# Kernel optimization log

Hardware: AMD Instinct MI355X
Metric: run time of the kernel (lower is better)

Reference implementation:

```python
import jax, jax.numpy as jnp
import numpy as np

DIM = 128
HOP = 2
NEIGH = [12, 2]  # neighbor_num per hop
ALPHA = 0.2      # leaky-relu slope
NUM_NODE = 50000
B, S = 128, 50
STDV = 1.0 / np.sqrt(DIM)


def _leaky(x):
    return jnp.where(x >= 0, x, ALPHA * x)


def _local_agg(h, adj, a_local):
    # h: [B,S,D], adj: [B,S,S] ints in 0..4, a_local: [4,D]
    a_in = h[:, :, None, :] * h[:, None, :, :]            # [B,S,S,D]
    e = _leaky(jnp.einsum('bijd,kd->kbij', a_in, a_local))  # [4,B,S,S]
    att = jnp.full(adj.shape, -9e15, dtype=h.dtype)
    for k in range(4):
        att = jnp.where(adj == k + 1, e[k], att)
    att = jax.nn.softmax(att, axis=-1)
    return jnp.einsum('bij,bjd->bid', att, h)


def _global_agg(self_v, neigh_v, extra_v, w1, w2, w3, bias):
    # self_v: [B,N,D], neigh_v: [B,N,K,D], extra_v: [B,N,D]
    a = _leaky(jnp.einsum('bnkd,de->bnke', extra_v[:, :, None, :] * neigh_v, w1))
    a = jnp.einsum('bnke,e->bnk', a, w2)
    a = jax.nn.softmax(a, axis=-1)
    agg = jnp.einsum('bnk,bnkd->bnd', a, neigh_v)
    out = jnp.concatenate([self_v, agg], axis=-1) @ w3 + bias
    return jax.nn.relu(out)


def setup_inputs() -> dict:
    key = jax.random.key(0)
    ks = jax.random.split(key, 12)
    u = lambda k, shp: jax.random.uniform(k, shp, jnp.float32, -STDV, STDV)
    return {
        'inputs': jax.random.randint(ks[0], (B, S), 0, NUM_NODE),
        'adj': jax.random.randint(ks[1], (B, S, S), 0, 5),
        'mask_item': jnp.ones((B, S), dtype=jnp.int32),
        'item': jax.random.randint(ks[2], (B, S), 0, NUM_NODE),
        'first_adj': jax.random.randint(ks[3], (B, S * NEIGH[0]), 0, NUM_NODE),
        'adj_all': jax.random.randint(ks[4], (NUM_NODE, 2), 0, NUM_NODE),
        'embedding': u(ks[5], (NUM_NODE, DIM)),
        'a_local': u(ks[6], (4, DIM)),
        'gw1': u(ks[7], (HOP, DIM, DIM)),
        'gw2': u(ks[8], (HOP, DIM)),
        'gw3': u(ks[9], (HOP, 2 * DIM, DIM)),
        'gbias': u(ks[10], (HOP, DIM)),
    }


def reference(inputs, adj, mask_item, item, first_adj, adj_all,
              embedding, a_local, gw1, gw2, gw3, gbias):
    b, s = inputs.shape
    h = embedding[inputs]                                  # [B,S,D]
    h_local = _local_agg(h, adj, a_local)

    m = mask_item.astype(embedding.dtype)[..., None]       # [B,S,1]
    item_emb = embedding[item] * m
    sum_item = jnp.sum(item_emb, 1) / jnp.sum(m, 1)        # [B,D]
    sess = sum_item[:, None, :]                            # [B,1,D]

    # multi-hop neighbor sampling
    neigh1 = first_adj.reshape(b, s * NEIGH[0])            # [B, 600]
    neigh2 = adj_all[neigh1.reshape(-1)].reshape(b, s * NEIGH[0] * NEIGH[1])  # [B,1200]
    ev = [embedding[inputs], embedding[neigh1], embedding[neigh2]]

    for n_hop in range(HOP):
        nxt = []
        for hop in range(HOP - n_hop):
            neigh_v = ev[hop + 1].reshape(b, -1, NEIGH[hop], DIM)
            extra_v = jnp.broadcast_to(sess, (b, ev[hop].shape[1], DIM))
            nxt.append(_global_agg(ev[hop], neigh_v, extra_v,
                                   gw1[n_hop], gw2[n_hop], gw3[n_hop], gbias[n_hop]))
        ev = nxt
    h_global = ev[0].reshape(b, s, DIM)

    # dropout is identity at eval
    return h_local + h_global
```

## Files before the change

kernel.cpp:

```cpp
#include <hip/hip_runtime.h>
#include <stdint.h>

typedef unsigned short ushort_t;
typedef __attribute__((ext_vector_type(8))) short bf16x8;
typedef __attribute__((ext_vector_type(4))) float f32x4;

#define B_   128
#define S_   50
#define D_   128
#define ALPHA_ 0.2f

__device__ __forceinline__ float bf2f(ushort_t u){
  return __uint_as_float(((uint32_t)u) << 16);
}
__device__ __forceinline__ ushort_t f2bf(float f){
  uint32_t x = __float_as_uint(f);
  x = (x + 0x7fffu + ((x >> 16) & 1u)) >> 16;
  return (ushort_t)x;
}
__device__ __forceinline__ float leaky(float x){ return x >= 0.f ? x : ALPHA_*x; }

__device__ __forceinline__ int detect_flag_block(const uint32_t* __restrict__ emb_raw){
  __shared__ int flg;
  if (threadIdx.x == 0){
    int ok = 1;
    for (int i = 0; i < 64; i++){
      uint32_t lo = emb_raw[i] & 0xffffu;
      uint32_t ex = (lo >> 7) & 0xFFu;
      if (!(lo == 0u || (ex >= 64u && ex <= 126u))) ok = 0;
    }
    flg = ok;
  }
  __syncthreads();
  return flg;
}

#define NLOCAL_ 512
#define NSESS_  64
#define NCVT_   3174
#define NPREP_  48
#define CVT_BASE_   (NLOCAL_ + NSESS_)
#define PREP_BASE_  (CVT_BASE_ + NCVT_)
#define K1_GRID_    (PREP_BASE_ + NPREP_)

__global__ __launch_bounds__(256) void k1(
    const int* __restrict__ inputs, const int* __restrict__ adj,
    const int* __restrict__ item, const int* __restrict__ mask,
    const void* __restrict__ p0, const void* __restrict__ p1,
    const void* __restrict__ p2, const void* __restrict__ p3,
    const void* __restrict__ p4, const void* __restrict__ p5,
    ushort_t* __restrict__ emb_b, uint4* __restrict__ w1f, uint4* __restrict__ w3f,
    ushort_t* __restrict__ sessb, ushort_t* __restrict__ hlb, int skip_emb)
{
  int blk = blockIdx.x, tid = threadIdx.x;
  int flag = detect_flag_block((const uint32_t*)p0);

  if (blk < NLOCAL_){
    __shared__ ushort_t hS[64][136];
    __shared__ float    attS[16][68];
    __shared__ int      sids[64];
    __shared__ ushort_t alS[512];
    int b  = blk >> 2;
    int mi = blk & 3;
    if (tid < 64) sids[tid] = (tid < S_) ? inputs[b*S_ + tid] : 0;
    for (int i = tid; i < 512; i += 256)
      alS[i] = flag ? ((const ushort_t*)p1)[i] : f2bf(((const float*)p1)[i]);
    __syncthreads();
    if (flag){
      const ushort_t* e16 = (const ushort_t*)p0;
      for (int idx = tid; idx < 64*16; idx += 256){
        int j = idx >> 4, ch = idx & 15;
        uint4 v = {0u, 0u, 0u, 0u};
        if (j < S_) v = *(const uint4*)(e16 + (size_t)sids[j]*D_ + ch*8);
        *(uint4*)(&hS[j][ch*8]) = v;
      }
    } else {
      const float* ef = (const float*)p0;
      for (int idx = tid; idx < 64*32; idx += 256){
        int j = idx >> 5, ch = idx & 31;
        union { ushort_t u[4]; uint2 d2; } o;
        o.d2 = make_uint2(0u, 0u);
        if (j < S_){
          float4 v = *(const float4*)(ef + (size_t)sids[j]*D_ + ch*4);
          o.u[0]=f2bf(v.x); o.u[1]=f2bf(v.y); o.u[2]=f2bf(v.z); o.u[3]=f2bf(v.w);
        }
        *(uint2*)(&hS[j][ch*4]) = o.d2;
      }
    }
    for (int idx = tid; idx < 16*64; idx += 256)
      attS[idx >> 6][idx & 63] = -9.0e15f;
    __syncthreads();

    int lane = tid & 63, wv = tid >> 6;
    int q = lane >> 4, c = lane & 15;

    f32x4 Eacc[4];
    #pragma unroll
    for (int ni = 0; ni < 4; ni++) Eacc[ni] = (f32x4){0.f,0.f,0.f,0.f};
    #pragma unroll
    for (int kt = 0; kt < 4; kt++){
      uint4 av = *(const uint4*)(alS + wv*D_ + kt*32 + q*8);
      const uint32_t* ap = (const uint32_t*)&av;
      uint4 hv = *(const uint4*)(&hS[mi*16 + c][kt*32 + q*8]);
      const uint32_t* hp = (const uint32_t*)&hv;
      union { ushort_t u[8]; bf16x8 v; } afr;
      #pragma unroll
      for (int p = 0; p < 4; p++){
        float x0 = __uint_as_float(hp[p] << 16)         * __uint_as_float(ap[p] << 16);
        float x1 = __uint_as_float(hp[p] & 0xffff0000u) * __uint_as_float(ap[p] & 0xffff0000u);
        afr.u[2*p]   = f2bf(x0);
        afr.u[2*p+1] = f2bf(x1);
      }
      #pragma unroll
      for (int ni = 0; ni < 4; ni++){
        union { uint4 q4; bf16x8 v; } bfr;
        bfr.q4 = *(const uint4*)(&hS[ni*16 + c][kt*32 + q*8]);
        Eacc[ni] = __builtin_amdgcn_mfma_f32_16x16x32_bf16(afr.v, bfr.v, Eacc[ni], 0,0,0);
      }
    }
    const int* adjb = adj + (size_t)b*S_*S_;
    #pragma unroll
    for (int ni = 0; ni < 4; ni++){
      int j = ni*16 + c;
      #pragma unroll
      for (int r = 0; r < 4; r++){
        int i = mi*16 + q*4 + r;
        if (i < S_ && j < S_){
          int kk = adjb[i*S_ + j];
          if (kk == wv + 1) attS[q*4 + r][j] = leaky(Eacc[ni][r]);
        }
      }
    }
    __syncthreads();
    {
      int r  = tid >> 4;
      int cg = tid & 15;
      int i  = mi*16 + r;
      float v0 = attS[r][cg*4+0], v1 = attS[r][cg*4+1];
      float v2 = attS[r][cg*4+2], v3 = attS[r][cg*4+3];
      float mx = fmaxf(fmaxf(v0,v1), fmaxf(v2,v3));
      #pragma unroll
      for (int off = 1; off < 16; off <<= 1) mx = fmaxf(mx, __shfl_xor(mx, off, 16));
      float e0 = (cg*4+0 < S_) ? __expf(v0 - mx) : 0.f;
      float e1 = (cg*4+1 < S_) ? __expf(v1 - mx) : 0.f;
      float e2 = (cg*4+2 < S_) ? __expf(v2 - mx) : 0.f;
      float e3 = (cg*4+3 < S_) ? __expf(v3 - mx) : 0.f;
      float s = e0 + e1 + e2 + e3;
      #pragma unroll
      for (int off = 1; off < 16; off <<= 1) s += __shfl_xor(s, off, 16);
      float inv = (i < S_) ? 1.f / s : 0.f;
      attS[r][cg*4+0] = e0*inv;
      attS[r][cg*4+1] = e1*inv;
      attS[r][cg*4+2] = e2*inv;
      attS[r][cg*4+3] = e3*inv;
    }
    __syncthreads();
    f32x4 Pacc[2];
    Pacc[0] = (f32x4){0.f,0.f,0.f,0.f};
    Pacc[1] = (f32x4){0.f,0.f,0.f,0.f};
    #pragma unroll
    for (int kt = 0; kt < 2; kt++){
      union { ushort_t u[8]; bf16x8 v; } afr;
      const float* arow = &attS[c][kt*32 + q*8];
      #pragma unroll
      for (int j = 0; j < 8; j++) afr.u[j] = f2bf(arow[j]);
      #pragma unroll
      for (int nn = 0; nn < 2; nn++){
        int ni = 2*wv + nn;
        union { ushort_t u[8]; bf16x8 v; } bfr;
        #pragma unroll
        for (int jj = 0; jj < 8; jj++)
          bfr.u[jj] = hS[kt*32 + q*8 + jj][ni*16 + c];
        Pacc[nn] = __builtin_amdgcn_mfma_f32_16x16x32_bf16(afr.v, bfr.v, Pacc[nn], 0,0,0);
      }
    }
    #pragma unroll
    for (int nn = 0; nn < 2; nn++){
      int d = (2*wv + nn)*16 + c;
      #pragma unroll
      for (int r = 0; r < 4; r++){
        int i = mi*16 + q*4 + r;
        if (i < S_) hlb[((size_t)b*S_ + i)*D_ + d] = f2bf(Pacc[nn][r]);
      }
    }
  } else if (blk < CVT_BASE_){
    int b = (blk - NLOCAL_)*2 + (tid >> 7);
    int d = tid & 127;
    float acc = 0.f, den = 0.f;
    if (flag){
      const ushort_t* e16 = (const ushort_t*)p0;
      for (int s = 0; s < S_; s++){
        float fm = (float)mask[b*S_ + s];
        int id = item[b*S_ + s];
        acc += fm * bf2f(e16[(size_t)id*D_ + d]);
        den += fm;
      }
    } else {
      const float* ef = (const float*)p0;
      for (int s = 0; s < S_; s++){
        float fm = (float)mask[b*S_ + s];
        int id = item[b*S_ + s];
        acc += fm * ef[(size_t)id*D_ + d];
        den += fm;
      }
    }
    sessb[b*D_ + d] = f2bf(acc / den);
  } else if (blk < PREP_BASE_){
    const int seg_end[6] = {6400000, 6400512, 6433280, 6433536, 6499072, 6499328};
    int base = ((blk - CVT_BASE_)*256 + tid) * 8;
    if (base >= 6499328) return;
    if (flag && skip_emb && base < 6400000) return;
    int s = 0;
    while (base >= seg_end[s]) s++;
    int segbase = (s == 0) ? 0 : seg_end[s-1];
    const void* src = (s==0)?p0:(s==1)?p1:(s==2)?p2:(s==3)?p3:(s==4)?p4:p5;
    int off = base - segbase;
    union { ushort_t u[8]; uint4 q4; } o;
    if (flag){
      o.q4 = *(const uint4*)((const ushort_t*)src + off);
    } else {
      const float* fp = (const float*)src + off;
      float4 v0 = *(const float4*)(fp);
      float4 v1 = *(const float4*)(fp + 4);
      o.u[0]=f2bf(v0.x); o.u[1]=f2bf(v0.y); o.u[2]=f2bf(v0.z); o.u[3]=f2bf(v0.w);
      o.u[4]=f2bf(v1.x); o.u[5]=f2bf(v1.y); o.u[6]=f2bf(v1.z); o.u[7]=f2bf(v1.w);
    }
    *(uint4*)(emb_b + base) = o.q4;
  } else {
    int id = (blk - PREP_BASE_)*256 + tid;
    if (id >= 12288) return;
    if (id < 4096){
      int h = id >> 11, i = id & 2047;
      int kt = i >> 9, rem = i & 511, t = rem >> 6, ln = rem & 63;
      int q = ln >> 4, c = ln & 15;
      union { ushort_t u[8]; uint4 q4; } e;
      #pragma unroll
      for (int j = 0; j < 8; j++){
        int idx = h*16384 + (32*kt + q*8 + j)*128 + 16*t + c;
        e.u[j] = flag ? ((const ushort_t*)p2)[idx] : f2bf(((const float*)p2)[idx]);
      }
      w1f[h*2048 + i] = e.q4;
    } else {
      int id2 = id - 4096;
      int h = id2 >> 12, i = id2 & 4095;
      int kt = i >> 9, rem = i & 511, t = rem >> 6, ln = rem & 63;
      int q = ln >> 4, c = ln & 15;
      union { ushort_t u[8]; uint4 q4; } e;
      #pragma unroll
      for (int j = 0; j < 8; j++){
        int idx = h*32768 + (32*kt + q*8 + j)*128 + 16*t + c;
        e.u[j] = flag ? ((const ushort_t*)p4)[idx] : f2bf(((const float*)p4)[idx]);
      }
      w3f[h*4096 + i] = e.q4;
    }
  }
}

#define NT2SCORE_ 768
#define NT2TPREP_ 392
#define K2_GRID_  (NT2SCORE_ + NT2TPREP_)

__global__ __launch_bounds__(256) void k2(
    const void* __restrict__ p0, const ushort_t* __restrict__ emb_b,
    const uint4* __restrict__ w3f,
    ushort_t* __restrict__ Tt, ushort_t* __restrict__ Tb,
    const ushort_t* __restrict__ sessb,
    const int* __restrict__ neigh1, const int* __restrict__ adj_all,
    const uint4* __restrict__ w1f, const ushort_t* __restrict__ w2,
    float* __restrict__ score)
{
  __shared__ uint4 frag[2048];
  __shared__ ushort_t sS[128];
  int blk = blockIdx.x, tid = threadIdx.x;
  int flag = detect_flag_block((const uint32_t*)p0);
  const ushort_t* emb = flag ? (const ushort_t*)p0 : emb_b;

  if (blk >= NT2SCORE_){
    int tp   = blk - NT2SCORE_;
    int half = tp & 1;
    int rowbase0 = (tp >> 1) * 256;
    for (int i = tid; i < 2048; i += 256) frag[i] = w3f[half*2048 + i];
    __syncthreads();
    int lane = tid & 63, wave = tid >> 6;
    int m = lane & 15, q = lane >> 4;
    ushort_t* Tdst = half ? Tb : Tt;
    #pragma unroll
    for (int rit = 0; rit < 4; rit++){
      int row = rowbase0 + rit*64 + wave*16 + m;
      int rowc = row < 50000 ? row : 49999;
      f32x4 acc[8];
      #pragma unroll
      for (int t = 0; t < 8; t++) acc[t] = (f32x4){0.f,0.f,0.f,0.f};
      #pragma unroll
      for (int kt = 0; kt < 4; kt++){
        union { uint4 q4; bf16x8 v; } bfr;
        bfr.q4 = *(const uint4*)(emb + (size_t)rowc*D_ + kt*32 + q*8);
        #pragma unroll
        for (int t = 0; t < 8; t++){
          union { uint4 q4; bf16x8 v; } af;
          af.q4 = frag[(kt*8 + t)*64 + lane];
          acc[t] = __builtin_amdgcn_mfma_f32_16x16x32_bf16(af.v, bfr.v, acc[t], 0, 0, 0);
        }
      }
      if (row < 50000){
        ushort_t* dst = Tdst + (size_t)row*D_;
        #pragma unroll
        for (int t = 0; t < 8; t++){
          int col0 = 16*t + q*4;
          union { ushort_t u[4]; uint2 d2; } pk;
          #pragma unroll
          for (int r = 0; r < 4; r++) pk.u[r] = f2bf(acc[t][r]);
          *(uint2*)(dst + col0) = pk.d2;
        }
      }
    }
    return;
  }

  int b2  = blk;
  int sb  = b2 / 6;
  int sub = b2 - sb*6;
  int grp = sub >> 1;
  int halft = sub & 1;
  if (tid < 16) ((uint4*)sS)[tid] = ((const uint4*)(sessb + (size_t)sb*D_))[tid];
  __syncthreads();
  for (int i = tid; i < 2048; i += 256){
    int kt = i >> 9, ln = i & 63, q = (ln >> 4);
    uint4 w = w1f[i];
    uint4 sv = *(const uint4*)(sS + kt*32 + q*8);
    const ushort_t* wu = (const ushort_t*)&w;
    const ushort_t* su = (const ushort_t*)&sv;
    union { ushort_t u[8]; uint4 q4; } o;
    #pragma unroll
    for (int j = 0; j < 8; j++) o.u[j] = f2bf(bf2f(wu[j]) * bf2f(su[j]));
    frag[i] = o.q4;
  }
  __syncthreads();
  int lane = tid & 63, wave = tid >> 6;
  int m = lane & 15, q = lane >> 4;
  float w2v[8];
  #pragma unroll
  for (int t = 0; t < 8; t++) w2v[t] = bf2f(w2[16*t + m]);

  int tend = halft ? 38 : 19;
  for (int t = halft*19 + wave; t < tend; t += 4){
    int rr = t*16 + m;
    int rrc = rr < 599 ? rr : 599;
    int nid;
    if (grp == 0){
      nid = neigh1[sb*600 + rrc];
    } else {
      int r2 = sb*1200 + (grp-1)*600 + rrc;
      nid = adj_all[(size_t)neigh1[r2 >> 1]*2 + (r2 & 1)];
    }
    const ushort_t* nrow = emb + (size_t)nid*D_;
    f32x4 acc[8];
    #pragma unroll
    for (int t8 = 0; t8 < 8; t8++) acc[t8] = (f32x4){0.f,0.f,0.f,0.f};
    #pragma unroll
    for (int kt = 0; kt < 4; kt++){
      union { uint4 q4; bf16x8 v; } af;
      af.q4 = *(const uint4*)(nrow + kt*32 + q*8);
      #pragma unroll
      for (int t8 = 0; t8 < 8; t8++){
        union { uint4 q4; bf16x8 v; } bf;
        bf.q4 = frag[(kt*8 + t8)*64 + lane];
        acc[t8] = __builtin_amdgcn_mfma_f32_16x16x32_bf16(af.v, bf.v, acc[t8], 0, 0, 0);
      }
    }
    #pragma unroll
    for (int r = 0; r < 4; r++){
      float s = 0.f;
      #pragma unroll
      for (int t8 = 0; t8 < 8; t8++) s += leaky(acc[t8][r]) * w2v[t8];
      s += __shfl_xor(s, 1, 64);
      s += __shfl_xor(s, 2, 64);
      s += __shfl_xor(s, 4, 64);
      s += __shfl_xor(s, 8, 64);
      if (m == 0){
        int rw = t*16 + q*4 + r;
        if (rw < 600){
          int sidx = (grp == 0) ? (sb*600 + rw)
                                : (76800 + sb*1200 + (grp-1)*600 + rw);
          score[sidx] = s;
        }
      }
    }
  }
}

__global__ __launch_bounds__(256) void score2_c(
    const ushort_t* __restrict__ sessb, const ushort_t* __restrict__ out1,
    const uint4* __restrict__ w1f, const ushort_t* __restrict__ w2,
    float* __restrict__ score)
{
  __shared__ uint4 bfrag[2048];
  __shared__ ushort_t sS[128];
  int blk = blockIdx.x, tid = threadIdx.x;
  int sb  = blk >> 2;
  int qtr = blk & 3;
  if (tid < 16) ((uint4*)sS)[tid] = ((const uint4*)(sessb + (size_t)sb*D_))[tid];
  __syncthreads();
  for (int i = tid; i < 2048; i += 256){
    int kt = i >> 9, ln = i & 63, q = (ln >> 4);
    uint4 w = w1f[i];
    uint4 sv = *(const uint4*)(sS + kt*32 + q*8);
    const ushort_t* wu = (const ushort_t*)&w;
    const ushort_t* su = (const ushort_t*)&sv;
    union { ushort_t u[8]; uint4 q4; } o;
    #pragma unroll
    for (int j = 0; j < 8; j++) o.u[j] = f2bf(bf2f(wu[j]) * bf2f(su[j]));
    bfrag[i] = o.q4;
  }
  __syncthreads();
  int lane = tid & 63, wave = tid >> 6;
  int m = lane & 15, q = lane >> 4;
  float w2v[8];
  #pragma unroll
  for (int t = 0; t < 8; t++) w2v[t] = bf2f(w2[16*t + m]);

  int t0 = qtr*10, tend = (qtr*10 + 10 < 38) ? qtr*10 + 10 : 38;
  for (int t = t0 + wave; t < tend; t += 4){
    int rr = t*16 + m;
    int rrc = rr < 599 ? rr : 599;
    const ushort_t* nrow = out1 + ((size_t)sb*600 + rrc)*D_;
    f32x4 acc[8];
    #pragma unroll
    for (int t8 = 0; t8 < 8; t8++) acc[t8] = (f32x4){0.f,0.f,0.f,0.f};
    #pragma unroll
    for (int kt = 0; kt < 4; kt++){
      union { uint4 q4; bf16x8 v; } af;
      af.q4 = *(const uint4*)(nrow + kt*32 + q*8);
      #pragma unroll
      for (int t8 = 0; t8 < 8; t8++){
        union { uint4 q4; bf16x8 v; } bf;
        bf.q4 = bfrag[(kt*8 + t8)*64 + lane];
        acc[t8] = __builtin_amdgcn_mfma_f32_16x16x32_bf16(af.v, bf.v, acc[t8], 0, 0, 0);
      }
    }
    #pragma unroll
    for (int r = 0; r < 4; r++){
      float s = 0.f;
      #pragma unroll
      for (int t8 = 0; t8 < 8; t8++) s += leaky(acc[t8][r]) * w2v[t8];
      s += __shfl_xor(s, 1, 64);
      s += __shfl_xor(s, 2, 64);
      s += __shfl_xor(s, 4, 64);
      s += __shfl_xor(s, 8, 64);
      if (m == 0){
        int rw = t*16 + q*4 + r;
        if (rw < 600) score[sb*600 + rw] = s;
      }
    }
  }
}

template<int K>
__device__ __forceinline__ void softmaxK(const float* __restrict__ sc, float att[K]){
  float mx = -__builtin_inff();
  #pragma unroll
  for (int k = 0; k < K; k++){ att[k] = sc[k]; mx = fmaxf(mx, att[k]); }
  float s = 0.f;
  #pragma unroll
  for (int k = 0; k < K; k++){ att[k] = __expf(att[k] - mx); s += att[k]; }
  float inv = 1.f / s;
  #pragma unroll
  for (int k = 0; k < K; k++) att[k] *= inv;
}

template<int K>
__device__ __forceinline__ void out_tile(
    int lane, const uint4* __restrict__ afrag,
    const ushort_t* __restrict__ sptr, const ushort_t* const nptr[K],
    const float att[K], f32x4 acc[8]){
  int q = lane >> 4;
  #pragma unroll
  for (int kt = 0; kt < 8; kt++){
    union { ushort_t u[8]; uint4 q4; bf16x8 v; } bfr;
    if (kt < 4){
      bfr.q4 = *(const uint4*)(sptr + kt*32 + q*8);
    } else {
      float g[8] = {0,0,0,0,0,0,0,0};
      #pragma unroll
      for (int k = 0; k < K; k++){
        uint4 nv = *(const uint4*)(nptr[k] + (kt-4)*32 + q*8);
        const uint32_t* np = (const uint32_t*)&nv;
        #pragma unroll
        for (int p = 0; p < 4; p++){
          g[2*p]   = fmaf(att[k], __uint_as_float(np[p] << 16),         g[2*p]);
// ... 12 lines not shown
  }
}

__global__ __launch_bounds__(256) void gather_out(
    const int* __restrict__ idx, const int* __restrict__ nbr,
    const int* __restrict__ adj_all, const float* __restrict__ score,
    const ushort_t* __restrict__ Tt, const ushort_t* __restrict__ Tb,
    const ushort_t* __restrict__ bias,
    ushort_t* __restrict__ o0c, ushort_t* __restrict__ out1c,
    int nA50, int nTot, int scoreBbase)
{
  int row  = (blockIdx.x*256 + threadIdx.x) >> 6;
  int lane = threadIdx.x & 63;
  if (row >= nTot) return;
  row = __builtin_amdgcn_readfirstlane(row);
  float b0 = bf2f(bias[lane*2]), b1 = bf2f(bias[lane*2 + 1]);
  float acc0, acc1;
  ushort_t* dst;
  if (row < nA50){
    float att[12];
    softmaxK<12>(score + (size_t)row*12, att);
    uint32_t sv = *(const uint32_t*)(Tt + (size_t)idx[row]*D_ + lane*2);
    acc0 = __uint_as_float(sv << 16);
    acc1 = __uint_as_float(sv & 0xffff0000u);
    #pragma unroll
    for (int k = 0; k < 12; k++){
      uint32_t nv = *(const uint32_t*)(Tb + (size_t)nbr[row*12 + k]*D_ + lane*2);
      acc0 = fmaf(att[k], __uint_as_float(nv << 16),          acc0);
      acc1 = fmaf(att[k], __uint_as_float(nv & 0xffff0000u),  acc1);
    }
    dst = o0c + (size_t)row*D_;
  } else {
    int rB = row - nA50;
    float att[2];
    softmaxK<2>(score + scoreBbase + (size_t)rB*2, att);
    int self = nbr[rB];
    uint32_t sv = *(const uint32_t*)(Tt + (size_t)self*D_ + lane*2);
    acc0 = __uint_as_float(sv << 16);
    acc1 = __uint_as_float(sv & 0xffff0000u);
    #pragma unroll
    for (int k = 0; k < 2; k++){
      uint32_t nv = *(const uint32_t*)(Tb + (size_t)adj_all[(size_t)self*2 + k]*D_ + lane*2);
      acc0 = fmaf(att[k], __uint_as_float(nv << 16),          acc0);
      acc1 = fmaf(att[k], __uint_as_float(nv & 0xffff0000u),  acc1);
    }
    dst = out1c + (size_t)rB*D_;
  }
  union { ushort_t u[2]; uint32_t d; } pk;
  pk.u[0] = f2bf(fmaxf(acc0 + b0, 0.f));
  pk.u[1] = f2bf(fmaxf(acc1 + b1, 0.f));
  *(uint32_t*)(dst + lane*2) = pk.d;
}

__global__ __launch_bounds__(256) void out_mfma_c2(
    const float* __restrict__ score, const ushort_t* __restrict__ out1,
    const ushort_t* __restrict__ selfsrc, const uint4* __restrict__ w3f,
    const ushort_t* __restrict__ bias,
    const ushort_t* __restrict__ addsrc, float* __restrict__ outf, int nrows){
  __shared__ uint4 afrag[4096];
  int tid = threadIdx.x;
  for (int i = tid; i < 4096; i += 256) afrag[i] = w3f[i];
  __syncthreads();
  int lane = tid & 63, wave = tid >> 6;
  int mrow = lane & 15, q = lane >> 4;
  float bv[8][4];
  #pragma unroll
  for (int t = 0; t < 8; t++){
    const ushort_t* bp = bias + 16*t + q*4;
    #pragma unroll
    for (int r = 0; r < 4; r++) bv[t][r] = bf2f(bp[r]);
  }
  int row_base = blockIdx.x*64 + wave*16;
  int row = row_base + mrow;
  bool active = row < nrows;
  int rowc = active ? row : (nrows - 1);
  const ushort_t* sptr = selfsrc + (size_t)rowc*D_;
  const ushort_t* nptr[12];
  #pragma unroll
  for (int k = 0; k < 12; k++) nptr[k] = out1 + (size_t)(rowc*12 + k)*D_;
  float att[12];
  softmaxK<12>(score + (size_t)rowc*12, att);
  f32x4 acc[8];
  #pragma unroll
  for (int t = 0; t < 8; t++) acc[t] = (f32x4){0.f,0.f,0.f,0.f};
  out_tile<12>(lane, afrag, sptr, nptr, att, acc);
  if (active){
    #pragma unroll
    for (int t = 0; t < 8; t++){
      int col0 = 16*t + q*4;
      float v[4];
      const ushort_t* ap = addsrc + (size_t)row*D_ + col0;
      #pragma unroll
      for (int r = 0; r < 4; r++)
        v[r] = fmaxf(acc[t][r] + bv[t][r], 0.f) + bf2f(ap[r]);
      *(f32x4*)(outf + (size_t)row*D_ + col0) = (f32x4){v[0], v[1], v[2], v[3]};
    }
  }
}

__global__ __launch_bounds__(256) void score_mfma_ab(
    const ushort_t* __restrict__ sessb, const ushort_t* __restrict__ emb,
    const int* __restrict__ neigh1, const int* __restrict__ adj_all,
    const uint4* __restrict__ w1f, const ushort_t* __restrict__ w2,
    float* __restrict__ score, int nA){
  __shared__ uint4 bfrag[2048];
  int tid = threadIdx.x;
  for (int i = tid; i < 2048; i += 256) bfrag[i] = w1f[i];
  __syncthreads();
  int lane = tid & 63, wave = tid >> 6;
  int m = lane & 15, q = lane >> 4;
  float w2v[8];
  #pragma unroll
  for (int t = 0; t < 8; t++) w2v[t] = bf2f(w2[16*t + m]);

  for (int it = 0; it < 2; it++){
    int row_base = blockIdx.x*128 + it*64 + wave*16;
    int row = row_base + m;
    const ushort_t* nrow; int b;
    if (row < nA){
      nrow = emb + (size_t)neigh1[row]*D_;
      b = row / 600;
    } else {
      int r2 = row - nA;
      nrow = emb + (size_t)adj_all[(size_t)neigh1[r2>>1]*2 + (r2&1)]*D_;
      b = r2 / 1200;
    }
    const ushort_t* srow = sessb + (size_t)b*D_;

    f32x4 acc[8];
    #pragma unroll
    for (int t = 0; t < 8; t++) acc[t] = (f32x4){0.f,0.f,0.f,0.f};
    #pragma unroll
    for (int kt = 0; kt < 4; kt++){
      uint4 nv = *(const uint4*)(nrow + kt*32 + q*8);
      uint4 sv = *(const uint4*)(srow + kt*32 + q*8);
      const uint32_t* np = (const uint32_t*)&nv;
      const uint32_t* sp = (const uint32_t*)&sv;
      union { ushort_t u[8]; bf16x8 v; } afr;
      #pragma unroll
      for (int p = 0; p < 4; p++){
        uint32_t n2 = np[p], s2 = sp[p];
        float a0 = __uint_as_float(n2 << 16)          * __uint_as_float(s2 << 16);
        float a1 = __uint_as_float(n2 & 0xffff0000u)  * __uint_as_float(s2 & 0xffff0000u);
        afr.u[2*p]   = f2bf(a0);
        afr.u[2*p+1] = f2bf(a1);
      }
      #pragma unroll
      for (int t = 0; t < 8; t++){
        union { uint4 q4; bf16x8 v; } bfr;
        bfr.q4 = bfrag[(kt*8 + t)*64 + lane];
// ... 157 lines not shown
  const ushort_t* nptr[12];
  #pragma unroll
  for (int k = 0; k < 12; k++) nptr[k] = out1 + (size_t)(rowc*12 + k)*D_;
  float att[12];
  softmaxK<12>(score + (size_t)rowc*12, att);
  f32x4 acc[8];
  #pragma unroll
  for (int t = 0; t < 8; t++) acc[t] = (f32x4){0.f,0.f,0.f,0.f};
  out_tile<12>(lane, afrag, sptr, nptr, att, acc);
  if (active){
    #pragma unroll
    for (int t = 0; t < 8; t++){
      int col0 = 16*t + q*4;
      float v[4];
      const ushort_t* ap = addsrc + (size_t)row*D_ + col0;
      #pragma unroll
      for (int r = 0; r < 4; r++)
        v[r] = fmaxf(acc[t][r] + bv[t][r], 0.f) + bf2f(ap[r]);
      *(f32x4*)(outf + (size_t)row*D_ + col0) = (f32x4){v[0], v[1], v[2], v[3]};
    }
  }
}

extern "C" void kernel_launch(void* const* d_in, const int* in_sizes, int n_in,
                              void* d_out, int out_size, void* d_ws, size_t ws_size,
                              hipStream_t stream) {
  const int* inputs    = (const int*)d_in[0];
  const int* adj       = (const int*)d_in[1];
  const int* mask_item = (const int*)d_in[2];
  const int* item      = (const int*)d_in[3];
  const int* first_adj = (const int*)d_in[4];
  const int* adj_all   = (const int*)d_in[5];

  char* ws = (char*)d_ws;
  size_t o = 0;
  ushort_t* emb_b  = (ushort_t*)(ws + o); o += 12800000;
  ushort_t* alocb  = (ushort_t*)(ws + o); o += 1024;
  ushort_t* gw1b   = (ushort_t*)(ws + o); o += 65536;
  ushort_t* gw2b   = (ushort_t*)(ws + o); o += 512;
  ushort_t* gw3b   = (ushort_t*)(ws + o); o += 131072;
  ushort_t* gbb    = (ushort_t*)(ws + o); o += 512;
  ushort_t* sessb  = (ushort_t*)(ws + o); o += 32768;
  ushort_t* hlb    = (ushort_t*)(ws + o); o += 1638400;
  uint4*    w1f    = (uint4*)(ws + o);    o += 65536;
  uint4*    w3f    = (uint4*)(ws + o);    o += 131072;
  size_t fixed = o;
  (void)alocb; (void)gw1b; (void)gw3b;

  float* outp = (float*)d_out;

  const size_t TPATH_NEED = fixed + 2*(size_t)12800000
                          + (size_t)128*153600
                          + (size_t)128*12800
                          + (size_t)3*128*600*4;
  bool tpath = (ws_size >= TPATH_NEED);

  k1<<<K1_GRID_, 256, 0, stream>>>(
      inputs, adj, item, mask_item,
      d_in[6], d_in[7], d_in[8], d_in[9], d_in[10], d_in[11],
      emb_b, w1f, w3f, sessb, hlb, tpath ? 1 : 0);

  if (tpath){
    ushort_t* Tt    = (ushort_t*)(ws + o);  o += 12800000;
    ushort_t* Tb    = (ushort_t*)(ws + o);  o += 12800000;
    ushort_t* out1c = (ushort_t*)(ws + o);  o += (size_t)128*153600;
    ushort_t* o0c   = (ushort_t*)(ws + o);  o += (size_t)128*12800;
    float*    score = (float*)(ws + o);
    int nA600 = 128*600, nA50 = 128*50, nTot = 128*650;

    k2<<<K2_GRID_, 256, 0, stream>>>(d_in[6], emb_b, w3f, Tt, Tb,
                                     sessb, first_adj, adj_all,
                                     w1f, gw2b, score);
    gather_out<<<(nTot*64 + 255)/256, 256, 0, stream>>>(inputs, first_adj, adj_all, score,
                                                        Tt, Tb, gbb, o0c, out1c,
                                                        nA50, nTot, nA600);
    score2_c<<<512, 256, 0, stream>>>(sessb, out1c, w1f + 2048, gw2b + 128, score);
    out_mfma_c2<<<(nA50 + 63)/64, 256, 0, stream>>>(score, out1c, o0c,
                                                    w3f + 4096, gbb + 128,
                                                    hlb, outp, nA50);
  } else {
    int CHB = 16;
    if      (ws_size >= fixed + (size_t)128*173600) CHB = 128;
    else if (ws_size >= fixed + (size_t)64 *173600) CHB = 64;
    else if (ws_size >= fixed + (size_t)32 *173600) CHB = 32;
    ushort_t* out1c = (ushort_t*)(ws + o);  o += (size_t)CHB*153600;
    ushort_t* o0c   = (ushort_t*)(ws + o);  o += (size_t)CHB*12800;
    float*    score = (float*)(ws + o);

    int nchunk = B_ / CHB;
    for (int c = 0; c < nchunk; c++){
      int b0 = c * CHB;
      const int* fadj  = first_adj + (size_t)b0 * 600;
      const ushort_t* sbc = sessb + (size_t)b0 * D_;
      ushort_t*  hlc   = hlb  + (size_t)b0 * 50 * D_;
      float*     outc  = outp + (size_t)b0 * 50 * D_;
      int nA600 = CHB*600, nA50 = CHB*50, nTot = CHB*650;

      score_mfma_ab<<<(3*nA600)/128, 256, 0, stream>>>(sbc, emb_b, fadj, adj_all,
                                                       w1f, gw2b, score, nA600);
      out_mfma_ab<<<(nTot + 127)/128, 512, 0, stream>>>(score, inputs + b0*50, fadj, adj_all,
                                                        emb_b, w3f, gbb, o0c, out1c,
                                                        nA50, nTot, nA600);
      score_mfma_c<<<nA600/128, 256, 0, stream>>>(sbc, out1c, w1f + 2048, gw2b + 128, score);
      out_mfma_c<<<(nA50 + 127)/128, 512, 0, stream>>>(score, out1c, o0c,
                                                       w3f + 4096, gbb + 128,
                                                       hlc, outc, nA50);
    }
  }
}
```

Baseline: 187.6 us.

## Move local attention blocks into score kernel and preload neighbor ids

```diff
diff --git a/kernel.cpp b/kernel.cpp
--- a/kernel.cpp
+++ b/kernel.cpp
@@ -35,13 +35,141 @@
   return flg;
 }
 
-#define NLOCAL_ 512
+__device__ void local_block(int b, int mi, int tid, int flag,
+    const int* __restrict__ inputs, const int* __restrict__ adj,
+    const void* __restrict__ p0, const void* __restrict__ p1,
+    ushort_t* __restrict__ hlb, uint4* smemU)
+{
+  ushort_t* hSp   = (ushort_t*)smemU;
+  float*    attSp = (float*)((char*)smemU + 17408);
+  int*      sidsp = (int*)((char*)smemU + 21760);
+  ushort_t* alSp  = (ushort_t*)((char*)smemU + 22016);
+  if (tid < 64) sidsp[tid] = (tid < S_) ? inputs[b*S_ + tid] : 0;
+  for (int i = tid; i < 512; i += 256)
+    alSp[i] = flag ? ((const ushort_t*)p1)[i] : f2bf(((const float*)p1)[i]);
+  __syncthreads();
+  if (flag){
+    const ushort_t* e16 = (const ushort_t*)p0;
+    for (int idx = tid; idx < 64*16; idx += 256){
+      int j = idx >> 4, ch = idx & 15;
+      uint4 v = {0u, 0u, 0u, 0u};
+      if (j < S_) v = *(const uint4*)(e16 + (size_t)sidsp[j]*D_ + ch*8);
+      *(uint4*)(hSp + j*136 + ch*8) = v;
+    }
+  } else {
+    const float* ef = (const float*)p0;
+    for (int idx = tid; idx < 64*32; idx += 256){
+      int j = idx >> 5, ch = idx & 31;
+      union { ushort_t u[4]; uint2 d2; } o;
+      o.d2 = make_uint2(0u, 0u);
+      if (j < S_){
+        float4 v = *(const float4*)(ef + (size_t)sidsp[j]*D_ + ch*4);
+        o.u[0]=f2bf(v.x); o.u[1]=f2bf(v.y); o.u[2]=f2bf(v.z); o.u[3]=f2bf(v.w);
+      }
+      *(uint2*)(hSp + j*136 + ch*4) = o.d2;
+    }
+  }
+  for (int idx = tid; idx < 16*64; idx += 256)
+    attSp[(idx >> 6)*68 + (idx & 63)] = -9.0e15f;
+  __syncthreads();
+
+  int lane = tid & 63, wv = tid >> 6;
+  int q = lane >> 4, c = lane & 15;
+
+  f32x4 Eacc[4];
+  #pragma unroll
+  for (int ni = 0; ni < 4; ni++) Eacc[ni] = (f32x4){0.f,0.f,0.f,0.f};
+  #pragma unroll
+  for (int kt = 0; kt < 4; kt++){
+    uint4 av = *(const uint4*)(alSp + wv*D_ + kt*32 + q*8);
+    const uint32_t* ap = (const uint32_t*)&av;
+    uint4 hv = *(const uint4*)(hSp + (mi*16 + c)*136 + kt*32 + q*8);
+    const uint32_t* hp = (const uint32_t*)&hv;
+    union { ushort_t u[8]; bf16x8 v; } afr;
+    #pragma unroll
+    for (int p = 0; p < 4; p++){
+      float x0 = __uint_as_float(hp[p] << 16)         * __uint_as_float(ap[p] << 16);
+      float x1 = __uint_as_float(hp[p] & 0xffff0000u) * __uint_as_float(ap[p] & 0xffff0000u);
+      afr.u[2*p]   = f2bf(x0);
+      afr.u[2*p+1] = f2bf(x1);
+    }
+    #pragma unroll
+    for (int ni = 0; ni < 4; ni++){
+      union { uint4 q4; bf16x8 v; } bfr;
+      bfr.q4 = *(const uint4*)(hSp + (ni*16 + c)*136 + kt*32 + q*8);
+      Eacc[ni] = __builtin_amdgcn_mfma_f32_16x16x32_bf16(afr.v, bfr.v, Eacc[ni], 0,0,0);
+    }
+  }
+  const int* adjb = adj + (size_t)b*S_*S_;
+  #pragma unroll
+  for (int ni = 0; ni < 4; ni++){
+    int j = ni*16 + c;
+    #pragma unroll
+    for (int r = 0; r < 4; r++){
+      int i = mi*16 + q*4 + r;
+      if (i < S_ && j < S_){
+        int kk = adjb[i*S_ + j];
+        if (kk == wv + 1) attSp[(q*4 + r)*68 + j] = leaky(Eacc[ni][r]);
+      }
+    }
+  }
+  __syncthreads();
+  {
+    int r  = tid >> 4;
+    int cg = tid & 15;
+    int i  = mi*16 + r;
+    float v0 = attSp[r*68 + cg*4+0], v1 = attSp[r*68 + cg*4+1];
+    float v2 = attSp[r*68 + cg*4+2], v3 = attSp[r*68 + cg*4+3];
+    float mx = fmaxf(fmaxf(v0,v1), fmaxf(v2,v3));
+    #pragma unroll
+    for (int off = 1; off < 16; off <<= 1) mx = fmaxf(mx, __shfl_xor(mx, off, 16));
+    float e0 = (cg*4+0 < S_) ? __expf(v0 - mx) : 0.f;
+    float e1 = (cg*4+1 < S_) ? __expf(v1 - mx) : 0.f;
+    float e2 = (cg*4+2 < S_) ? __expf(v2 - mx) : 0.f;
+    float e3 = (cg*4+3 < S_) ? __expf(v3 - mx) : 0.f;
+    float s = e0 + e1 + e2 + e3;
+    #pragma unroll
+    for (int off = 1; off < 16; off <<= 1) s += __shfl_xor(s, off, 16);
+    float inv = (i < S_) ? 1.f / s : 0.f;
+    attSp[r*68 + cg*4+0] = e0*inv;
+    attSp[r*68 + cg*4+1] = e1*inv;
+    attSp[r*68 + cg*4+2] = e2*inv;
+    attSp[r*68 + cg*4+3] = e3*inv;
+  }
+  __syncthreads();
+  f32x4 Pacc[2];
+  Pacc[0] = (f32x4){0.f,0.f,0.f,0.f};
+  Pacc[1] = (f32x4){0.f,0.f,0.f,0.f};
+  #pragma unroll
+  for (int kt = 0; kt < 2; kt++){
+    union { ushort_t u[8]; bf16x8 v; } afr;
+    const float* arow = attSp + c*68 + kt*32 + q*8;
+    #pragma unroll
+    for (int j = 0; j < 8; j++) afr.u[j] = f2bf(arow[j]);
+    #pragma unroll
+    for (int nn = 0; nn < 2; nn++){
+      int ni = 2*wv + nn;
+      union { ushort_t u[8]; bf16x8 v; } bfr;
+      #pragma unroll
+      for (int jj = 0; jj < 8; jj++)
+        bfr.u[jj] = hSp[(kt*32 + q*8 + jj)*136 + ni*16 + c];
+      Pacc[nn] = __builtin_amdgcn_mfma_f32_16x16x32_bf16(afr.v, bfr.v, Pacc[nn], 0,0,0);
+    }
+  }
+  #pragma unroll
+  for (int nn = 0; nn < 2; nn++){
+    int d = (2*wv + nn)*16 + c;
+    #pragma unroll
+    for (int r = 0; r < 4; r++){
+      int i = mi*16 + q*4 + r;
+      if (i < S_) hlb[((size_t)b*S_ + i)*D_ + d] = f2bf(Pacc[nn][r]);
+    }
+  }
+}
+
 #define NSESS_  64
 #define NCVT_   3174
 #define NPREP_  48
-#define CVT_BASE_   (NLOCAL_ + NSESS_)
-#define PREP_BASE_  (CVT_BASE_ + NCVT_)
-#define K1_GRID_    (PREP_BASE_ + NPREP_)
 
 __global__ __launch_bounds__(256) void k1(
     const int* __restrict__ inputs, const int* __restrict__ adj,
@@ -50,141 +178,20 @@
     const void* __restrict__ p2, const void* __restrict__ p3,
     const void* __restrict__ p4, const void* __restrict__ p5,
     ushort_t* __restrict__ emb_b, uint4* __restrict__ w1f, uint4* __restrict__ w3f,
-    ushort_t* __restrict__ sessb, ushort_t* __restrict__ hlb, int skip_emb)
+    ushort_t* __restrict__ sessb, ushort_t* __restrict__ hlb,
+    int nlocal, int skip_emb)
 {
+  __shared__ uint4 smemU[1440];
   int blk = blockIdx.x, tid = threadIdx.x;
   int flag = detect_flag_block((const uint32_t*)p0);
 
-  if (blk < NLOCAL_){
-    __shared__ ushort_t hS[64][136];
-    __shared__ float    attS[16][68];
-    __shared__ int      sids[64];
-    __shared__ ushort_t alS[512];
-    int b  = blk >> 2;
-    int mi = blk & 3;
-    if (tid < 64) sids[tid] = (tid < S_) ? inputs[b*S_ + tid] : 0;
-    for (int i = tid; i < 512; i += 256)
-      alS[i] = flag ? ((const ushort_t*)p1)[i] : f2bf(((const float*)p1)[i]);
-    __syncthreads();
-    if (flag){
-      const ushort_t* e16 = (const ushort_t*)p0;
-      for (int idx = tid; idx < 64*16; idx += 256){
-        int j = idx >> 4, ch = idx & 15;
-        uint4 v = {0u, 0u, 0u, 0u};
-        if (j < S_) v = *(const uint4*)(e16 + (size_t)sids[j]*D_ + ch*8);
-        *(uint4*)(&hS[j][ch*8]) = v;
-      }
-    } else {
-      const float* ef = (const float*)p0;
-      for (int idx = tid; idx < 64*32; idx += 256){
-        int j = idx >> 5, ch = idx & 31;
-        union { ushort_t u[4]; uint2 d2; } o;
-        o.d2 = make_uint2(0u, 0u);
-        if (j < S_){
-          float4 v = *(const float4*)(ef + (size_t)sids[j]*D_ + ch*4);
-          o.u[0]=f2bf(v.x); o.u[1]=f2bf(v.y); o.u[2]=f2bf(v.z); o.u[3]=f2bf(v.w);
-        }
-        *(uint2*)(&hS[j][ch*4]) = o.d2;
-      }
-    }
-    for (int idx = tid; idx < 16*64; idx += 256)
-      attS[idx >> 6][idx & 63] = -9.0e15f;
-    __syncthreads();
-
-    int lane = tid & 63, wv = tid >> 6;
-    int q = lane >> 4, c = lane & 15;
-
-    f32x4 Eacc[4];
-    #pragma unroll
-    for (int ni = 0; ni < 4; ni++) Eacc[ni] = (f32x4){0.f,0.f,0.f,0.f};
-    #pragma unroll
-    for (int kt = 0; kt < 4; kt++){
-      uint4 av = *(const uint4*)(alS + wv*D_ + kt*32 + q*8);
-      const uint32_t* ap = (const uint32_t*)&av;
-      uint4 hv = *(const uint4*)(&hS[mi*16 + c][kt*32 + q*8]);
-      const uint32_t* hp = (const uint32_t*)&hv;
-      union { ushort_t u[8]; bf16x8 v; } afr;
-      #pragma unroll
-      for (int p = 0; p < 4; p++){
-        float x0 = __uint_as_float(hp[p] << 16)         * __uint_as_float(ap[p] << 16);
-        float x1 = __uint_as_float(hp[p] & 0xffff0000u) * __uint_as_float(ap[p] & 0xffff0000u);
-        afr.u[2*p]   = f2bf(x0);
-        afr.u[2*p+1] = f2bf(x1);
-      }
-      #pragma unroll
-      for (int ni = 0; ni < 4; ni++){
-        union { uint4 q4; bf16x8 v; } bfr;
-        bfr.q4 = *(const uint4*)(&hS[ni*16 + c][kt*32 + q*8]);
-        Eacc[ni] = __builtin_amdgcn_mfma_f32_16x16x32_bf16(afr.v, bfr.v, Eacc[ni], 0,0,0);
-      }
-    }
-    const int* adjb = adj + (size_t)b*S_*S_;
-    #pragma unroll
-    for (int ni = 0; ni < 4; ni++){
-      int j = ni*16 + c;
-      #pragma unroll
-      for (int r = 0; r < 4; r++){
-        int i = mi*16 + q*4 + r;
-        if (i < S_ && j < S_){
-          int kk = adjb[i*S_ + j];
-          if (kk == wv + 1) attS[q*4 + r][j] = leaky(Eacc[ni][r]);
-        }
-      }
-    }
-    __syncthreads();
-    {
-      int r  = tid >> 4;
-      int cg = tid & 15;
-      int i  = mi*16 + r;
-      float v0 = attS[r][cg*4+0], v1 = attS[r][cg*4+1];
-      float v2 = attS[r][cg*4+2], v3 = attS[r][cg*4+3];
-      float mx = fmaxf(fmaxf(v0,v1), fmaxf(v2,v3));
-      #pragma unroll
-      for (int off = 1; off < 16; off <<= 1) mx = fmaxf(mx, __shfl_xor(mx, off, 16));
-      float e0 = (cg*4+0 < S_) ? __expf(v0 - mx) : 0.f;
-      float e1 = (cg*4+1 < S_) ? __expf(v1 - mx) : 0.f;
-      float e2 = (cg*4+2 < S_) ? __expf(v2 - mx) : 0.f;
-      float e3 = (cg*4+3 < S_) ? __expf(v3 - mx) : 0.f;
-      float s = e0 + e1 + e2 + e3;
-      #pragma unroll
-      for (int off = 1; off < 16; off <<= 1) s += __shfl_xor(s, off, 16);
-      float inv = (i < S_) ? 1.f / s : 0.f;
-      attS[r][cg*4+0] = e0*inv;
-      attS[r][cg*4+1] = e1*inv;
-      attS[r][cg*4+2] = e2*inv;
-      attS[r][cg*4+3] = e3*inv;
-    }
-    __syncthreads();
-    f32x4 Pacc[2];
-    Pacc[0] = (f32x4){0.f,0.f,0.f,0.f};
-    Pacc[1] = (f32x4){0.f,0.f,0.f,0.f};
-    #pragma unroll
-    for (int kt = 0; kt < 2; kt++){
-      union { ushort_t u[8]; bf16x8 v; } afr;
-      const float* arow = &attS[c][kt*32 + q*8];
-      #pragma unroll
-      for (int j = 0; j < 8; j++) afr.u[j] = f2bf(arow[j]);
-      #pragma unroll
-      for (int nn = 0; nn < 2; nn++){
-        int ni = 2*wv + nn;
-        union { ushort_t u[8]; bf16x8 v; } bfr;
-        #pragma unroll
-        for (int jj = 0; jj < 8; jj++)
-          bfr.u[jj] = hS[kt*32 + q*8 + jj][ni*16 + c];
-        Pacc[nn] = __builtin_amdgcn_mfma_f32_16x16x32_bf16(afr.v, bfr.v, Pacc[nn], 0,0,0);
-      }
-    }
-    #pragma unroll
-    for (int nn = 0; nn < 2; nn++){
-      int d = (2*wv + nn)*16 + c;
-      #pragma unroll
-      for (int r = 0; r < 4; r++){
-        int i = mi*16 + q*4 + r;
-        if (i < S_) hlb[((size_t)b*S_ + i)*D_ + d] = f2bf(Pacc[nn][r]);
-      }
-    }
-  } else if (blk < CVT_BASE_){
-    int b = (blk - NLOCAL_)*2 + (tid >> 7);
+  if (blk < nlocal){
+    local_block(blk >> 2, blk & 3, tid, flag, inputs, adj, p0, p1, hlb, smemU);
+    return;
+  }
+  int b2 = blk - nlocal;
+  if (b2 < NSESS_){
+    int b = b2*2 + (tid >> 7);
     int d = tid & 127;
     float acc = 0.f, den = 0.f;
     if (flag){
@@ -205,9 +212,9 @@
       }
     }
     sessb[b*D_ + d] = f2bf(acc / den);
-  } else if (blk < PREP_BASE_){
+  } else if (b2 < NSESS_ + NCVT_){
     const int seg_end[6] = {6400000, 6400512, 6433280, 6433536, 6499072, 6499328};
-    int base = ((blk - CVT_BASE_)*256 + tid) * 8;
+    int base = ((b2 - NSESS_)*256 + tid) * 8;
     if (base >= 6499328) return;
     if (flag && skip_emb && base < 6400000) return;
     int s = 0;
@@ -227,7 +234,7 @@
     }
     *(uint4*)(emb_b + base) = o.q4;
   } else {
-    int id = (blk - PREP_BASE_)*256 + tid;
+    int id = (b2 - NSESS_ - NCVT_)*256 + tid;
     if (id >= 12288) return;
     if (id < 4096){
       int h = id >> 11, i = id & 2047;
@@ -271,6 +278,7 @@
 {
   __shared__ uint4 frag[2048];
   __shared__ ushort_t sS[128];
+  __shared__ int nidS[304];
   int blk = blockIdx.x, tid = threadIdx.x;
   int flag = detect_flag_block((const uint32_t*)p0);
   const ushort_t* emb = flag ? (const ushort_t*)p0 : emb_b;
@@ -322,8 +330,21 @@
   int sub = b2 - sb*6;
   int grp = sub >> 1;
   int halft = sub & 1;
+  int rbase = halft * 304;
   if (tid < 16) ((uint4*)sS)[tid] = ((const uint4*)(sessb + (size_t)sb*D_))[tid];
   __syncthreads();
+  for (int i = tid; i < 304; i += 256){
+    int rr = rbase + i;
+    int rrc = rr < 599 ? rr : 599;
+    int nid;
+    if (grp == 0){
+      nid = neigh1[sb*600 + rrc];
+    } else {
+      int r2 = sb*1200 + (grp-1)*600 + rrc;
+      nid = adj_all[(size_t)neigh1[r2 >> 1]*2 + (r2 & 1)];
+    }
+    nidS[i] = nid;
+  }
   for (int i = tid; i < 2048; i += 256){
     int kt = i >> 9, ln = i & 63, q = (ln >> 4);
     uint4 w = w1f[i];
@@ -344,15 +365,7 @@
 
   int tend = halft ? 38 : 19;
   for (int t = halft*19 + wave; t < tend; t += 4){
-    int rr = t*16 + m;
-    int rrc = rr < 599 ? rr : 599;
-    int nid;
-    if (grp == 0){
-      nid = neigh1[sb*600 + rrc];
-    } else {
-      int r2 = sb*1200 + (grp-1)*600 + rrc;
-      nid = adj_all[(size_t)neigh1[r2 >> 1]*2 + (r2 & 1)];
-    }
+    int nid = nidS[t*16 + m - rbase];
     const ushort_t* nrow = emb + (size_t)nid*D_;
     f32x4 acc[8];
     #pragma unroll
@@ -389,16 +402,27 @@
   }
 }
 
-__global__ __launch_bounds__(256) void score2_c(
+__global__ __launch_bounds__(256) void score_local(
+    const int* __restrict__ inputs, const int* __restrict__ adj,
+    const void* __restrict__ p0, const void* __restrict__ p1,
+    ushort_t* __restrict__ hlb,
     const ushort_t* __restrict__ sessb, const ushort_t* __restrict__ out1,
     const uint4* __restrict__ w1f, const ushort_t* __restrict__ w2,
     float* __restrict__ score)
 {
-  __shared__ uint4 bfrag[2048];
-  __shared__ ushort_t sS[128];
+  __shared__ uint4 smemU[2080];
   int blk = blockIdx.x, tid = threadIdx.x;
-  int sb  = blk >> 2;
-  int qtr = blk & 3;
+  int flag = detect_flag_block((const uint32_t*)p0);
+
+  if (blk < 512){
+    local_block(blk >> 2, blk & 3, tid, flag, inputs, adj, p0, p1, hlb, smemU);
+    return;
+  }
+  uint4*    bfrag = smemU;
+  ushort_t* sS    = (ushort_t*)(smemU + 2048);
+  int b2  = blk - 512;
+  int sb  = b2 >> 2;
+  int qtr = b2 & 3;
   if (tid < 16) ((uint4*)sS)[tid] = ((const uint4*)(sessb + (size_t)sb*D_))[tid];
   __syncthreads();
   for (int i = tid; i < 2048; i += 256){
@@ -863,11 +887,6 @@
                           + (size_t)3*128*600*4;
   bool tpath = (ws_size >= TPATH_NEED);
 
-  k1<<<K1_GRID_, 256, 0, stream>>>(
-      inputs, adj, item, mask_item,
-      d_in[6], d_in[7], d_in[8], d_in[9], d_in[10], d_in[11],
-      emb_b, w1f, w3f, sessb, hlb, tpath ? 1 : 0);
-
   if (tpath){
     ushort_t* Tt    = (ushort_t*)(ws + o);  o += 12800000;
     ushort_t* Tb    = (ushort_t*)(ws + o);  o += 12800000;
@@ -876,13 +895,19 @@
     float*    score = (float*)(ws + o);
     int nA600 = 128*600, nA50 = 128*50, nTot = 128*650;
 
+    k1<<<NSESS_ + NCVT_ + NPREP_, 256, 0, stream>>>(
+        inputs, adj, item, mask_item,
+        d_in[6], d_in[7], d_in[8], d_in[9], d_in[10], d_in[11],
+        emb_b, w1f, w3f, sessb, hlb, 0, 1);
+
     k2<<<K2_GRID_, 256, 0, stream>>>(d_in[6], emb_b, w3f, Tt, Tb,
                                      sessb, first_adj, adj_all,
                                      w1f, gw2b, score);
     gather_out<<<(nTot*64 + 255)/256, 256, 0, stream>>>(inputs, first_adj, adj_all, score,
                                                         Tt, Tb, gbb, o0c, out1c,
                                                         nA50, nTot, nA600);
-    score2_c<<<512, 256, 0, stream>>>(sessb, out1c, w1f + 2048, gw2b + 128, score);
+    score_local<<<1024, 256, 0, stream>>>(inputs, adj, d_in[6], d_in[7], hlb,
+                                          sessb, out1c, w1f + 2048, gw2b + 128, score);
     out_mfma_c2<<<(nA50 + 63)/64, 256, 0, stream>>>(score, out1c, o0c,
                                                     w3f + 4096, gbb + 128,
                                                     hlb, outp, nA50);
@@ -895,6 +920,11 @@
     ushort_t* o0c   = (ushort_t*)(ws + o);  o += (size_t)CHB*12800;
     float*    score = (float*)(ws + o);
 
+    k1<<<512 + NSESS_ + NCVT_ + NPREP_, 256, 0, stream>>>(
+        inputs, adj, item, mask_item,
+        d_in[6], d_in[7], d_in[8], d_in[9], d_in[10], d_in[11],
+        emb_b, w1f, w3f, sessb, hlb, 512, 0);
+
     int nchunk = B_ / CHB;
     for (int c = 0; c < nchunk; c++){
       int b0 = c * CHB;
```

Result: slower. 197.4 us (+5.2%).

## Precompute hop-2 W3 projections and apply attention after the linear layer

Applied to the files above, without the earlier changes.

```diff
diff --git a/kernel.cpp b/kernel.cpp
--- a/kernel.cpp
+++ b/kernel.cpp
@@ -271,6 +271,7 @@
 {
   __shared__ uint4 frag[2048];
   __shared__ ushort_t sS[128];
+  __shared__ int nidS[304];
   int blk = blockIdx.x, tid = threadIdx.x;
   int flag = detect_flag_block((const uint32_t*)p0);
   const ushort_t* emb = flag ? (const ushort_t*)p0 : emb_b;
@@ -322,8 +323,21 @@
   int sub = b2 - sb*6;
   int grp = sub >> 1;
   int halft = sub & 1;
+  int rbase = halft * 304;
   if (tid < 16) ((uint4*)sS)[tid] = ((const uint4*)(sessb + (size_t)sb*D_))[tid];
   __syncthreads();
+  for (int i = tid; i < 304; i += 256){
+    int rr = rbase + i;
+    int rrc = rr < 599 ? rr : 599;
+    int nid;
+    if (grp == 0){
+      nid = neigh1[sb*600 + rrc];
+    } else {
+      int r2 = sb*1200 + (grp-1)*600 + rrc;
+      nid = adj_all[(size_t)neigh1[r2 >> 1]*2 + (r2 & 1)];
+    }
+    nidS[i] = nid;
+  }
   for (int i = tid; i < 2048; i += 256){
     int kt = i >> 9, ln = i & 63, q = (ln >> 4);
     uint4 w = w1f[i];
@@ -344,15 +358,7 @@
 
   int tend = halft ? 38 : 19;
   for (int t = halft*19 + wave; t < tend; t += 4){
-    int rr = t*16 + m;
-    int rrc = rr < 599 ? rr : 599;
-    int nid;
-    if (grp == 0){
-      nid = neigh1[sb*600 + rrc];
-    } else {
-      int r2 = sb*1200 + (grp-1)*600 + rrc;
-      nid = adj_all[(size_t)neigh1[r2 >> 1]*2 + (r2 & 1)];
-    }
+    int nid = nidS[t*16 + m - rbase];
     const ushort_t* nrow = emb + (size_t)nid*D_;
     f32x4 acc[8];
     #pragma unroll
@@ -389,35 +395,79 @@
   }
 }
 
-__global__ __launch_bounds__(256) void score2_c(
+#define K4SCORE_ 512
+#define K4TB_    300
+#define K4TT_    25
+#define K4_GRID_ (K4SCORE_ + K4TB_ + K4TT_)
+
+__global__ __launch_bounds__(256) void k4(
     const ushort_t* __restrict__ sessb, const ushort_t* __restrict__ out1,
-    const uint4* __restrict__ w1f, const ushort_t* __restrict__ w2,
-    float* __restrict__ score)
+    const ushort_t* __restrict__ o0c,
+    const uint4* __restrict__ w1f_h1, const ushort_t* __restrict__ w2_h1,
+    const uint4* __restrict__ w3f_h1,
+    float* __restrict__ score, float* __restrict__ Tb1f, float* __restrict__ Tt1f)
 {
-  __shared__ uint4 bfrag[2048];
+  __shared__ uint4 frag[2048];
   __shared__ ushort_t sS[128];
   int blk = blockIdx.x, tid = threadIdx.x;
-  int sb  = blk >> 2;
-  int qtr = blk & 3;
+
+  if (blk >= K4SCORE_){
+    int tp = blk - K4SCORE_;
+    const ushort_t* src; float* dst; const uint4* fragsrc; int rowbase;
+    if (tp < K4TB_){ src = out1; dst = Tb1f; fragsrc = w3f_h1 + 2048; rowbase = tp*256; }
+    else           { src = o0c;  dst = Tt1f; fragsrc = w3f_h1;        rowbase = (tp - K4TB_)*256; }
+    for (int i = tid; i < 2048; i += 256) frag[i] = fragsrc[i];
+    __syncthreads();
+    int lane = tid & 63, wave = tid >> 6;
+    int m = lane & 15, q = lane >> 4;
+    #pragma unroll
+    for (int rit = 0; rit < 4; rit++){
+      int row = rowbase + rit*64 + wave*16 + m;
+      f32x4 acc[8];
+      #pragma unroll
+      for (int t = 0; t < 8; t++) acc[t] = (f32x4){0.f,0.f,0.f,0.f};
+      #pragma unroll
+      for (int kt = 0; kt < 4; kt++){
+        union { uint4 q4; bf16x8 v; } bfr;
+        bfr.q4 = *(const uint4*)(src + (size_t)row*D_ + kt*32 + q*8);
+        #pragma unroll
+        for (int t = 0; t < 8; t++){
+          union { uint4 q4; bf16x8 v; } af;
+          af.q4 = frag[(kt*8 + t)*64 + lane];
+          acc[t] = __builtin_amdgcn_mfma_f32_16x16x32_bf16(af.v, bfr.v, acc[t], 0, 0, 0);
+        }
+      }
+      #pragma unroll
+      for (int t = 0; t < 8; t++){
+        int col0 = 16*t + q*4;
+        *(f32x4*)(dst + (size_t)row*D_ + col0) = acc[t];
+      }
+    }
+    return;
+  }
+
+  int b2  = blk;
+  int sb  = b2 >> 2;
+  int qtr = b2 & 3;
   if (tid < 16) ((uint4*)sS)[tid] = ((const uint4*)(sessb + (size_t)sb*D_))[tid];
   __syncthreads();
   for (int i = tid; i < 2048; i += 256){
     int kt = i >> 9, ln = i & 63, q = (ln >> 4);
-    uint4 w = w1f[i];
+    uint4 w = w1f_h1[i];
     uint4 sv = *(const uint4*)(sS + kt*32 + q*8);
     const ushort_t* wu = (const ushort_t*)&w;
     const ushort_t* su = (const ushort_t*)&sv;
     union { ushort_t u[8]; uint4 q4; } o;
     #pragma unroll
     for (int j = 0; j < 8; j++) o.u[j] = f2bf(bf2f(wu[j]) * bf2f(su[j]));
-    bfrag[i] = o.q4;
+    frag[i] = o.q4;
   }
   __syncthreads();
   int lane = tid & 63, wave = tid >> 6;
   int m = lane & 15, q = lane >> 4;
   float w2v[8];
   #pragma unroll
-  for (int t = 0; t < 8; t++) w2v[t] = bf2f(w2[16*t + m]);
+  for (int t = 0; t < 8; t++) w2v[t] = bf2f(w2_h1[16*t + m]);
 
   int t0 = qtr*10, tend = (qtr*10 + 10 < 38) ? qtr*10 + 10 : 38;
   for (int t = t0 + wave; t < tend; t += 4){
@@ -434,7 +484,7 @@
       #pragma unroll
       for (int t8 = 0; t8 < 8; t8++){
         union { uint4 q4; bf16x8 v; } bf;
-        bf.q4 = bfrag[(kt*8 + t8)*64 + lane];
+        bf.q4 = frag[(kt*8 + t8)*64 + lane];
         acc[t8] = __builtin_amdgcn_mfma_f32_16x16x32_bf16(af.v, bf.v, acc[t8], 0, 0, 0);
       }
     }
@@ -553,50 +603,31 @@
   *(uint32_t*)(dst + lane*2) = pk.d;
 }
 
-__global__ __launch_bounds__(256) void out_mfma_c2(
-    const float* __restrict__ score, const ushort_t* __restrict__ out1,
-    const ushort_t* __restrict__ selfsrc, const uint4* __restrict__ w3f,
-    const ushort_t* __restrict__ bias,
-    const ushort_t* __restrict__ addsrc, float* __restrict__ outf, int nrows){
-  __shared__ uint4 afrag[4096];
-  int tid = threadIdx.x;
-  for (int i = tid; i < 4096; i += 256) afrag[i] = w3f[i];
-  __syncthreads();
-  int lane = tid & 63, wave = tid >> 6;
-  int mrow = lane & 15, q = lane >> 4;
-  float bv[8][4];
-  #pragma unroll
-  for (int t = 0; t < 8; t++){
-    const ushort_t* bp = bias + 16*t + q*4;
-    #pragma unroll
-    for (int r = 0; r < 4; r++) bv[t][r] = bf2f(bp[r]);
-  }
-  int row_base = blockIdx.x*64 + wave*16;
-  int row = row_base + mrow;
-  bool active = row < nrows;
-  int rowc = active ? row : (nrows - 1);
-  const ushort_t* sptr = selfsrc + (size_t)rowc*D_;
-  const ushort_t* nptr[12];
-  #pragma unroll
-  for (int k = 0; k < 12; k++) nptr[k] = out1 + (size_t)(rowc*12 + k)*D_;
+__global__ __launch_bounds__(256) void final_c(
+    const float* __restrict__ score, const float* __restrict__ Tt1f,
+    const float* __restrict__ Tb1f, const ushort_t* __restrict__ bias,
+    const ushort_t* __restrict__ hl, float* __restrict__ outp, int nrows)
+{
+  int row  = (blockIdx.x*256 + threadIdx.x) >> 6;
+  int lane = threadIdx.x & 63;
+  if (row >= nrows) return;
+  row = __builtin_amdgcn_readfirstlane(row);
+  int c0 = lane*2;
   float att[12];
-  softmaxK<12>(score + (size_t)rowc*12, att);
-  f32x4 acc[8];
-  #pragma unroll
-  for (int t = 0; t < 8; t++) acc[t] = (f32x4){0.f,0.f,0.f,0.f};
-  out_tile<12>(lane, afrag, sptr, nptr, att, acc);
-  if (active){
-    #pragma unroll
-    for (int t = 0; t < 8; t++){
-      int col0 = 16*t + q*4;
-      float v[4];
-      const ushort_t* ap = addsrc + (size_t)row*D_ + col0;
-      #pragma unroll
-      for (int r = 0; r < 4; r++)
-        v[r] = fmaxf(acc[t][r] + bv[t][r], 0.f) + bf2f(ap[r]);
-      *(f32x4*)(outf + (size_t)row*D_ + col0) = (f32x4){v[0], v[1], v[2], v[3]};
-    }
-  }
+  softmaxK<12>(score + (size_t)row*12, att);
+  float acc0 = Tt1f[(size_t)row*D_ + c0];
+  float acc1 = Tt1f[(size_t)row*D_ + c0 + 1];
+  #pragma unroll
+  for (int k = 0; k < 12; k++){
+    const float* tb = Tb1f + (size_t)(row*12 + k)*D_ + c0;
+    acc0 = fmaf(att[k], tb[0], acc0);
+    acc1 = fmaf(att[k], tb[1], acc1);
+  }
+  float b0 = bf2f(bias[c0]), b1 = bf2f(bias[c0 + 1]);
+  float v0 = fmaxf(acc0 + b0, 0.f) + bf2f(hl[(size_t)row*D_ + c0]);
+  float v1 = fmaxf(acc1 + b1, 0.f) + bf2f(hl[(size_t)row*D_ + c0 + 1]);
+  float2 o2; o2.x = v0; o2.y = v1;
+  *(float2*)(outp + (size_t)row*D_ + c0) = o2;
 }
 
 __global__ __launch_bounds__(256) void score_mfma_ab(
@@ -860,7 +891,9 @@
   const size_t TPATH_NEED = fixed + 2*(size_t)12800000
                           + (size_t)128*153600
                           + (size_t)128*12800
-                          + (size_t)3*128*600*4;
+                          + (size_t)3*128*600*4
+                          + (size_t)76800*512
+                          + (size_t)6400*512;
   bool tpath = (ws_size >= TPATH_NEED);
 
   k1<<<K1_GRID_, 256, 0, stream>>>(
@@ -873,7 +906,9 @@
     ushort_t* Tb    = (ushort_t*)(ws + o);  o += 12800000;
     ushort_t* out1c = (ushort_t*)(ws + o);  o += (size_t)128*153600;
     ushort_t* o0c   = (ushort_t*)(ws + o);  o += (size_t)128*12800;
-    float*    score = (float*)(ws + o);
+    float*    score = (float*)(ws + o);     o += (size_t)3*128*600*4;
+    float*    Tb1f  = (float*)(ws + o);     o += (size_t)76800*512;
+    float*    Tt1f  = (float*)(ws + o);     o += (size_t)6400*512;
     int nA600 = 128*600, nA50 = 128*50, nTot = 128*650;
 
     k2<<<K2_GRID_, 256, 0, stream>>>(d_in[6], emb_b, w3f, Tt, Tb,
@@ -882,10 +917,11 @@
     gather_out<<<(nTot*64 + 255)/256, 256, 0, stream>>>(inputs, first_adj, adj_all, score,
                                                         Tt, Tb, gbb, o0c, out1c,
                                                         nA50, nTot, nA600);
-    score2_c<<<512, 256, 0, stream>>>(sessb, out1c, w1f + 2048, gw2b + 128, score);
-    out_mfma_c2<<<(nA50 + 63)/64, 256, 0, stream>>>(score, out1c, o0c,
-                                                    w3f + 4096, gbb + 128,
-                                                    hlb, outp, nA50);
+    k4<<<K4_GRID_, 256, 0, stream>>>(sessb, out1c, o0c,
+                                     w1f + 2048, gw2b + 128, w3f + 4096,
+                                     score, Tb1f, Tt1f);
+    final_c<<<(nA50*64 + 255)/256, 256, 0, stream>>>(score, Tt1f, Tb1f,
+                                                     gbb + 128, hlb, outp, nA50);
   } else {
     int CHB = 16;
     if      (ws_size >= fixed + (size_t)128*173600) CHB = 128;
```

New measurement: 192.6 us. 1.03x slower.
